# Kernel optimization log

Hardware: AMD Instinct MI355X
Metric: run time of the kernel (lower is better)

Reference implementation:

```python
import jax, jax.numpy as jnp
import numpy as np

N_NODES = 20000
N_EDGES = 320000
IN_CH = 64
OUT_CH = 64
HEADS = 4
NEG_SLOPE = 0.2
BN_EPS = 1e-5


def setup_inputs() -> dict:
    key = jax.random.key(0)
    ks = jax.random.split(key, 12)
    x = jax.random.normal(ks[0], (N_NODES, IN_CH), dtype=jnp.float32)
    embedding = jax.random.normal(ks[1], (N_NODES, OUT_CH), dtype=jnp.float32)
    # random edges guaranteed to have no self loops (module removes them anyway)
    src = jax.random.randint(ks[2], (N_EDGES,), 0, N_NODES, dtype=jnp.int32)
    off = jax.random.randint(ks[3], (N_EDGES,), 1, N_NODES, dtype=jnp.int32)
    dst = (src + off) % N_NODES
    edge_index = jnp.stack([src, dst], axis=0)  # [2, E]
    glorot = lambda k, shape: jax.random.uniform(k, shape, jnp.float32, -1.0, 1.0) * np.sqrt(6.0 / (shape[-2] * shape[-1] if len(shape) > 1 else shape[-1]))
    W = glorot(ks[4], (IN_CH, HEADS * OUT_CH))            # lin weight (no bias)
    att_i = glorot(ks[5], (1, HEADS, OUT_CH))
    att_j = glorot(ks[6], (1, HEADS, OUT_CH))
    att_em_i = glorot(ks[7], (1, HEADS, OUT_CH)) * 0.1    # zeros at init; random for test coverage
    att_em_j = glorot(ks[8], (1, HEADS, OUT_CH)) * 0.1
    bias = jnp.zeros((OUT_CH,), jnp.float32)
    gamma = jnp.ones((OUT_CH,), jnp.float32)
    beta = jnp.zeros((OUT_CH,), jnp.float32)
    return {"x": x, "edge_index": edge_index, "embedding": embedding, "W": W,
            "att_i": att_i, "att_j": att_j, "att_em_i": att_em_i, "att_em_j": att_em_j,
            "bias": bias, "gamma": gamma, "beta": beta}


def _gnn_forward(x, edge_index, embedding, W, att_i, att_j, att_em_i, att_em_j,
                 bias, gamma, beta):
    N = x.shape[0]
    H, C = att_i.shape[1], att_i.shape[2]
    # add self loops (input edges contain none by construction)
    loops = jnp.arange(N, dtype=edge_index.dtype)
    src = jnp.concatenate([edge_index[0], loops])  # x_j / embedding_j index
    dst = jnp.concatenate([edge_index[1], loops])  # x_i / embedding_i index (edge_index_i)
    xl = (x @ W).reshape(N, H, C)                  # [N,H,C]
    # attention logits decompose per node: <x, att> + <emb, att_em>
    logit_i = jnp.einsum('nhc,hc->nh', xl, att_i[0]) + jnp.einsum('nc,hc->nh', embedding, att_em_i[0])
    logit_j = jnp.einsum('nhc,hc->nh', xl, att_j[0]) + jnp.einsum('nc,hc->nh', embedding, att_em_j[0])
    alpha = logit_i[dst] + logit_j[src]            # [Etot,H]
    alpha = jnp.where(alpha >= 0, alpha, NEG_SLOPE * alpha)  # leaky_relu
    # segment softmax over destination node (PyG softmax)
    amax = jax.ops.segment_max(alpha, dst, num_segments=N)   # every node has a self loop
    alpha = jnp.exp(alpha - amax[dst])
    denom = jax.ops.segment_sum(alpha, dst, num_segments=N)
    alpha = alpha / (denom[dst] + 1e-16)
    # weighted message aggregation (scatter-add)
    msg = alpha[:, :, None] * xl[src]              # [Etot,H,C]
    out = jax.ops.segment_sum(msg, dst, num_segments=N)      # [N,H,C]
    out = out.mean(axis=1) + bias                  # concat=False -> head mean
    # BatchNorm1d (training-mode batch statistics) + ReLU
    mu = out.mean(axis=0)
    var = jnp.mean((out - mu) ** 2, axis=0)
    out = (out - mu) * jax.lax.rsqrt(var + BN_EPS) * gamma + beta
    return jax.nn.relu(out)


def reference(x, edge_index, embedding, W, att_i, att_j, att_em_i, att_em_j, bias, gamma, beta):
    return _gnn_forward(x, edge_index, embedding, W, att_i, att_j, att_em_i, att_em_j, bias, gamma, beta)
```

## Files before the change

kernel.cpp:

```cpp
#include <hip/hip_runtime.h>
#include <hip/hip_fp16.h>
#include <math.h>

#define N_NODES 20000
#define N_EDGES 320000
#define N_TOT (N_EDGES + N_NODES)
#define IN_CH 64
#define OUT_CH 64
#define HEADS 4
#define HC (HEADS * OUT_CH)
#define NEG_SLOPE 0.2f
#define BN_EPS 1e-5f
#define BN_SLOTS 64
#define CAP 64
#define XL_BLOCKS (N_NODES / 16)

__global__ __launch_bounds__(256) void k_xl(
    const float* __restrict__ x, const float* __restrict__ W,
    const float* __restrict__ emb, const float* __restrict__ att_i,
    const float* __restrict__ att_j, const float* __restrict__ att_em_i,
    const float* __restrict__ att_em_j, const int* __restrict__ srcA,
    const int* __restrict__ dstA, __half* __restrict__ xlh,
    float* __restrict__ logit_i, float* __restrict__ logit_j,
    int* __restrict__ cnt, int* __restrict__ bS, float* __restrict__ bnp) {
    __shared__ float xs[16][64];
    const int t = threadIdx.x;
    const int lane = t & 63, w = t >> 6;
    const int node0 = blockIdx.x * 16;
    const int gtid = blockIdx.x * 256 + t;

    if (gtid < BN_SLOTS * 128) bnp[gtid] = 0.f;

    {
        int n = t >> 4, c4 = (t & 15) * 4;
        float4 v = *(const float4*)&x[(node0 + n) * IN_CH + c4];
        *(float4*)&xs[n][c4] = v;
    }
    const float ai = att_i[t], aj = att_j[t];
    const float aei = att_em_i[t], aej = att_em_j[t];
    __syncthreads();

    const unsigned B = (unsigned)cnt[N_NODES];
    int s0, d0, p0;
    {
        const int e0 = gtid;
        if (e0 < N_EDGES) {
            s0 = srcA[e0];
            d0 = dstA[e0];
        } else {
            s0 = d0 = e0 - N_EDGES;
        }
        p0 = atomicAdd(&cnt[d0], 1);
    }
    const bool has1 = (gtid < N_TOT - XL_BLOCKS * 256);
    int p1 = 0;
    if (has1) p1 = atomicAdd(&cnt[gtid], 1);

    float acc[16];
#pragma unroll
    for (int n = 0; n < 16; ++n) acc[n] = 0.f;
#pragma unroll 1
    for (int kt = 0; kt < 4; ++kt) {
        float wt[16];
#pragma unroll
        for (int k = 0; k < 16; ++k) wt[k] = W[(kt * 16 + k) * HC + t];
#pragma unroll
        for (int n = 0; n < 16; ++n) {
            const float4* xr = (const float4*)&xs[n][kt * 16];
#pragma unroll
            for (int k4 = 0; k4 < 4; ++k4) {
                float4 xv = xr[k4];
                acc[n] += xv.x * wt[4 * k4] + xv.y * wt[4 * k4 + 1] +
                          xv.z * wt[4 * k4 + 2] + xv.w * wt[4 * k4 + 3];
            }
        }
    }

#pragma unroll
    for (int n = 0; n < 16; ++n) {
        const int gn = node0 + n;
        xlh[gn * HC + t] = __float2half(acc[n]);
        float e = emb[gn * OUT_CH + lane];
        float li = acc[n] * ai + e * aei;
        float lj = acc[n] * aj + e * aej;
#pragma unroll
        for (int o = 32; o > 0; o >>= 1) {
            li += __shfl_xor(li, o, 64);
            lj += __shfl_xor(lj, o, 64);
        }
        if (lane == 0) {
            logit_i[gn * HEADS + w] = li;
            logit_j[gn * HEADS + w] = lj;
        }
    }

    {
        unsigned pos = (unsigned)p0 - B;
        if (pos < CAP) bS[d0 * CAP + (int)pos] = s0;
    }
    if (has1) {
        unsigned pos = (unsigned)p1 - B;
        if (pos < CAP) bS[gtid * CAP + (int)pos] = gtid;
    }
}

__global__ __launch_bounds__(256) void k_node(
    const __half* __restrict__ xlh, const int* __restrict__ cnt,
    const int* __restrict__ bS, const float* __restrict__ logit_i,
    const float* __restrict__ logit_j, const float* __restrict__ bias,
    float* __restrict__ tmp, float* __restrict__ bnp) {
    const int t = threadIdx.x;
    const int wv = t >> 6, lane = t & 63;
    const int n = blockIdx.x * 4 + wv;
    const unsigned B = (unsigned)cnt[N_NODES];
    const int m = min((int)((unsigned)cnt[n] - B), CAP);
    const int h = lane >> 4;
    const int nb = n * CAP;
    const float li = logit_i[n * HEADS + h];

    float4 acc = {0.f, 0.f, 0.f, 0.f};
    float ssum = 0.f;

#pragma unroll 8
    for (int i = 0; i < m; ++i) {
        int s = bS[nb + i];
        float a = li + logit_j[s * HEADS + h];
        a = (a >= 0.f) ? a : NEG_SLOPE * a;
        float wgt = __expf(a);
        ushort4 r = *(const ushort4*)(xlh + (size_t)s * HC + lane * 4);
        ssum += wgt;
        acc.x += wgt * __half2float(__ushort_as_half(r.x));
        acc.y += wgt * __half2float(__ushort_as_half(r.y));
        acc.z += wgt * __half2float(__ushort_as_half(r.z));
        acc.w += wgt * __half2float(__ushort_as_half(r.w));
    }
    const float inv = 1.f / ssum;
    acc.x *= inv; acc.y *= inv; acc.z *= inv; acc.w *= inv;
#pragma unroll
    for (int o = 16; o <= 32; o <<= 1) {
        acc.x += __shfl_xor(acc.x, o, 64);
        acc.y += __shfl_xor(acc.y, o, 64);
        acc.z += __shfl_xor(acc.z, o, 64);
        acc.w += __shfl_xor(acc.w, o, 64);
    }
    __shared__ float rows[4][64];
    if (lane < 16) {
        int c = lane * 4;
        float4 b = *(const float4*)&bias[c];
        float4 o4 = {0.25f * acc.x + b.x, 0.25f * acc.y + b.y,
                     0.25f * acc.z + b.z, 0.25f * acc.w + b.w};
        *(float4*)&tmp[n * OUT_CH + c] = o4;
        *(float4*)&rows[wv][c] = o4;
    }
    __syncthreads();
    if (t < 64) {
        float s = 0.f, ss = 0.f;
#pragma unroll
        for (int r = 0; r < 4; ++r) {
            float v = rows[r][t];
            s += v;
            ss += v * v;
        }
        int slot = (blockIdx.x & (BN_SLOTS - 1)) * 128;
        atomicAdd(&bnp[slot + t], s);
        atomicAdd(&bnp[slot + 64 + t], ss);
    }
}

__global__ __launch_bounds__(256) void k_final(const float* __restrict__ tmp,
                                               const float* __restrict__ bnp,
                                               const float* __restrict__ gamma,
                                               const float* __restrict__ beta,
                                               float* __restrict__ out) {
    __shared__ float sscale[64], sshift[64];
    const int t = threadIdx.x;
    if (t < 64) {
        float s = 0.f, ss = 0.f;
#pragma unroll
        for (int k = 0; k < BN_SLOTS; ++k) {
            s += bnp[k * 128 + t];
            ss += bnp[k * 128 + 64 + t];
        }
        const float invN = 1.f / (float)N_NODES;
        float mu = s * invN;
        float var = ss * invN - mu * mu;
        float sc = rsqrtf(var + BN_EPS) * gamma[t];
        sscale[t] = sc;
        sshift[t] = beta[t] - mu * sc;
    }
    __syncthreads();
    const float4* t4 = (const float4*)tmp;
    float4* o4 = (float4*)out;
    const int total4 = N_NODES * OUT_CH / 4;
    for (int i = blockIdx.x * 256 + t; i < total4; i += gridDim.x * 256) {
        int c = (i & 15) * 4;
        float4 v = t4[i];
        float4 r;
        r.x = fmaxf(v.x * sscale[c] + sshift[c], 0.f);
        r.y = fmaxf(v.y * sscale[c + 1] + sshift[c + 1], 0.f);
        r.z = fmaxf(v.z * sscale[c + 2] + sshift[c + 2], 0.f);
        r.w = fmaxf(v.w * sscale[c + 3] + sshift[c + 3], 0.f);
        o4[i] = r;
    }
}

extern "C" void kernel_launch(void* const* d_in, const int* in_sizes, int n_in,
                              void* d_out, int out_size, void* d_ws,
                              size_t ws_size, hipStream_t stream) {
    const float* x = (const float*)d_in[0];
    const int* ei = (const int*)d_in[1];
    const float* emb = (const float*)d_in[2];
    const float* W = (const float*)d_in[3];
    const float* att_i = (const float*)d_in[4];
    const float* att_j = (const float*)d_in[5];
    const float* att_em_i = (const float*)d_in[6];
    const float* att_em_j = (const float*)d_in[7];
    const float* bias = (const float*)d_in[8];
    const float* gamma = (const float*)d_in[9];
    const float* beta = (const float*)d_in[10];
    float* out = (float*)d_out;

    const int* srcA = ei;
    const int* dstA = ei + N_EDGES;

    char* p = (char*)d_ws;
    auto alloc = [&](size_t bytes) {
        char* r = p;
        p += (bytes + 255) & ~size_t(255);
        return r;
    };
    __half* xlh = (__half*)alloc(sizeof(__half) * N_NODES * HC);
    float* lgi = (float*)alloc(sizeof(float) * N_NODES * HEADS);
    float* lgj = (float*)alloc(sizeof(float) * N_NODES * HEADS);
    float* tmp = (float*)alloc(sizeof(float) * N_NODES * OUT_CH);
    float* bnp = (float*)alloc(sizeof(float) * BN_SLOTS * 128);
    int* cnt = (int*)alloc(sizeof(int) * (N_NODES + 1));
    int* bS = (int*)alloc(sizeof(int) * N_NODES * CAP);
    (void)alloc(4096);

    k_xl<<<XL_BLOCKS, 256, 0, stream>>>(x, W, emb, att_i, att_j, att_em_i,
                                        att_em_j, srcA, dstA, xlh, lgi, lgj,
                                        cnt, bS, bnp);
    k_node<<<N_NODES / 4, 256, 0, stream>>>(xlh, cnt, bS, lgi, lgj, bias, tmp,
                                            bnp);
    k_final<<<256, 256, 0, stream>>>(tmp, bnp, gamma, beta, out);
}
```

Measured before the change: 162.6 us.

## Replicate edge-bucket counters across block groups to cut atomic contention

```diff
diff --git a/kernel.cpp b/kernel.cpp
--- a/kernel.cpp
+++ b/kernel.cpp
@@ -12,7 +12,9 @@
 #define NEG_SLOPE 0.2f
 #define BN_EPS 1e-5f
 #define BN_SLOTS 64
-#define CAP 64
+#define NREP 8
+#define SUBCAP 16
+#define CSTRIDE (N_NODES + 1)
 #define XL_BLOCKS (N_NODES / 16)
 
 __global__ __launch_bounds__(256) void k_xl(
@@ -28,6 +30,8 @@
     const int lane = t & 63, w = t >> 6;
     const int node0 = blockIdx.x * 16;
     const int gtid = blockIdx.x * 256 + t;
+    const int rid = blockIdx.x & (NREP - 1);
+    int* __restrict__ cntR = cnt + rid * CSTRIDE;
 
     if (gtid < BN_SLOTS * 128) bnp[gtid] = 0.f;
 
@@ -39,22 +43,6 @@
     const float ai = att_i[t], aj = att_j[t];
     const float aei = att_em_i[t], aej = att_em_j[t];
     __syncthreads();
-
-    const unsigned B = (unsigned)cnt[N_NODES];
-    int s0, d0, p0;
-    {
-        const int e0 = gtid;
-        if (e0 < N_EDGES) {
-            s0 = srcA[e0];
-            d0 = dstA[e0];
-        } else {
-            s0 = d0 = e0 - N_EDGES;
-        }
-        p0 = atomicAdd(&cnt[d0], 1);
-    }
-    const bool has1 = (gtid < N_TOT - XL_BLOCKS * 256);
-    int p1 = 0;
-    if (has1) p1 = atomicAdd(&cnt[gtid], 1);
 
     float acc[16];
 #pragma unroll
@@ -75,6 +63,17 @@
             }
         }
     }
+
+    const unsigned B = (unsigned)cntR[N_NODES];
+    int s0, d0, p0;
+    {
+        s0 = srcA[gtid];
+        d0 = dstA[gtid];
+        p0 = atomicAdd(&cntR[d0], 1);
+    }
+    const bool has1 = (gtid < N_NODES);
+    int p1 = 0;
+    if (has1) p1 = atomicAdd(&cntR[gtid], 1);
 
 #pragma unroll
     for (int n = 0; n < 16; ++n) {
@@ -96,11 +95,13 @@
 
     {
         unsigned pos = (unsigned)p0 - B;
-        if (pos < CAP) bS[d0 * CAP + (int)pos] = s0;
+        if (pos < SUBCAP)
+            bS[(d0 * NREP + rid) * SUBCAP + (int)pos] = s0;
     }
     if (has1) {
         unsigned pos = (unsigned)p1 - B;
-        if (pos < CAP) bS[gtid * CAP + (int)pos] = gtid;
+        if (pos < SUBCAP)
+            bS[(gtid * NREP + rid) * SUBCAP + (int)pos] = gtid;
     }
 }
 
@@ -112,27 +113,30 @@
     const int t = threadIdx.x;
     const int wv = t >> 6, lane = t & 63;
     const int n = blockIdx.x * 4 + wv;
-    const unsigned B = (unsigned)cnt[N_NODES];
-    const int m = min((int)((unsigned)cnt[n] - B), CAP);
     const int h = lane >> 4;
-    const int nb = n * CAP;
     const float li = logit_i[n * HEADS + h];
 
     float4 acc = {0.f, 0.f, 0.f, 0.f};
     float ssum = 0.f;
 
-#pragma unroll 8
-    for (int i = 0; i < m; ++i) {
-        int s = bS[nb + i];
-        float a = li + logit_j[s * HEADS + h];
-        a = (a >= 0.f) ? a : NEG_SLOPE * a;
-        float wgt = __expf(a);
-        ushort4 r = *(const ushort4*)(xlh + (size_t)s * HC + lane * 4);
-        ssum += wgt;
-        acc.x += wgt * __half2float(__ushort_as_half(r.x));
-        acc.y += wgt * __half2float(__ushort_as_half(r.y));
-        acc.z += wgt * __half2float(__ushort_as_half(r.z));
-        acc.w += wgt * __half2float(__ushort_as_half(r.w));
+#pragma unroll 1
+    for (int r = 0; r < NREP; ++r) {
+        const int cbase = r * CSTRIDE;
+        const unsigned B = (unsigned)cnt[cbase + N_NODES];
+        const int m = min((int)((unsigned)cnt[cbase + n] - B), SUBCAP);
+        const int nb = (n * NREP + r) * SUBCAP;
+        for (int i = 0; i < m; ++i) {
+            int s = bS[nb + i];
+            float a = li + logit_j[s * HEADS + h];
+            a = (a >= 0.f) ? a : NEG_SLOPE * a;
+            float wgt = __expf(a);
+            ushort4 rr = *(const ushort4*)(xlh + (size_t)s * HC + lane * 4);
+            ssum += wgt;
+            acc.x += wgt * __half2float(__ushort_as_half(rr.x));
+            acc.y += wgt * __half2float(__ushort_as_half(rr.y));
+            acc.z += wgt * __half2float(__ushort_as_half(rr.z));
+            acc.w += wgt * __half2float(__ushort_as_half(rr.w));
+        }
     }
     const float inv = 1.f / ssum;
     acc.x *= inv; acc.y *= inv; acc.z *= inv; acc.w *= inv;
@@ -234,8 +238,8 @@
     float* lgj = (float*)alloc(sizeof(float) * N_NODES * HEADS);
     float* tmp = (float*)alloc(sizeof(float) * N_NODES * OUT_CH);
     float* bnp = (float*)alloc(sizeof(float) * BN_SLOTS * 128);
-    int* cnt = (int*)alloc(sizeof(int) * (N_NODES + 1));
-    int* bS = (int*)alloc(sizeof(int) * N_NODES * CAP);
+    int* cnt = (int*)alloc(sizeof(int) * NREP * CSTRIDE);
+    int* bS = (int*)alloc(sizeof(int) * N_NODES * NREP * SUBCAP);
     (void)alloc(4096);
 
     k_xl<<<XL_BLOCKS, 256, 0, stream>>>(x, W, emb, att_i, att_j, att_em_i,
```

After: 181.5 us. +11.6%, slower.

## Halve nodes per block in projection kernel and move edge atomics after GEMM

Applied to the files above, without the earlier changes.

```diff
diff --git a/kernel.cpp b/kernel.cpp
--- a/kernel.cpp
+++ b/kernel.cpp
@@ -13,7 +13,8 @@
 #define BN_EPS 1e-5f
 #define BN_SLOTS 64
 #define CAP 64
-#define XL_BLOCKS (N_NODES / 16)
+#define NPB 8
+#define XL_BLOCKS (N_NODES / NPB)
 
 __global__ __launch_bounds__(256) void k_xl(
     const float* __restrict__ x, const float* __restrict__ W,
@@ -23,15 +24,15 @@
     const int* __restrict__ dstA, __half* __restrict__ xlh,
     float* __restrict__ logit_i, float* __restrict__ logit_j,
     int* __restrict__ cnt, int* __restrict__ bS, float* __restrict__ bnp) {
-    __shared__ float xs[16][64];
+    __shared__ float xs[NPB][64];
     const int t = threadIdx.x;
     const int lane = t & 63, w = t >> 6;
-    const int node0 = blockIdx.x * 16;
+    const int node0 = blockIdx.x * NPB;
     const int gtid = blockIdx.x * 256 + t;
 
     if (gtid < BN_SLOTS * 128) bnp[gtid] = 0.f;
 
-    {
+    if (t < NPB * 16) {
         int n = t >> 4, c4 = (t & 15) * 4;
         float4 v = *(const float4*)&x[(node0 + n) * IN_CH + c4];
         *(float4*)&xs[n][c4] = v;
@@ -40,32 +41,16 @@
     const float aei = att_em_i[t], aej = att_em_j[t];
     __syncthreads();
 
-    const unsigned B = (unsigned)cnt[N_NODES];
-    int s0, d0, p0;
-    {
-        const int e0 = gtid;
-        if (e0 < N_EDGES) {
-            s0 = srcA[e0];
-            d0 = dstA[e0];
-        } else {
-            s0 = d0 = e0 - N_EDGES;
-        }
-        p0 = atomicAdd(&cnt[d0], 1);
-    }
-    const bool has1 = (gtid < N_TOT - XL_BLOCKS * 256);
-    int p1 = 0;
-    if (has1) p1 = atomicAdd(&cnt[gtid], 1);
-
-    float acc[16];
-#pragma unroll
-    for (int n = 0; n < 16; ++n) acc[n] = 0.f;
+    float acc[NPB];
+#pragma unroll
+    for (int n = 0; n < NPB; ++n) acc[n] = 0.f;
 #pragma unroll 1
     for (int kt = 0; kt < 4; ++kt) {
         float wt[16];
 #pragma unroll
         for (int k = 0; k < 16; ++k) wt[k] = W[(kt * 16 + k) * HC + t];
 #pragma unroll
-        for (int n = 0; n < 16; ++n) {
+        for (int n = 0; n < NPB; ++n) {
             const float4* xr = (const float4*)&xs[n][kt * 16];
 #pragma unroll
             for (int k4 = 0; k4 < 4; ++k4) {
@@ -76,8 +61,21 @@
         }
     }
 
-#pragma unroll
-    for (int n = 0; n < 16; ++n) {
+    const unsigned B = (unsigned)cnt[N_NODES];
+    const bool hasE = (gtid < N_TOT);
+    int s0 = 0, d0 = 0, p0 = 0;
+    if (hasE) {
+        if (gtid < N_EDGES) {
+            s0 = srcA[gtid];
+            d0 = dstA[gtid];
+        } else {
+            s0 = d0 = gtid - N_EDGES;
+        }
+        p0 = atomicAdd(&cnt[d0], 1);
+    }
+
+#pragma unroll
+    for (int n = 0; n < NPB; ++n) {
         const int gn = node0 + n;
         xlh[gn * HC + t] = __float2half(acc[n]);
         float e = emb[gn * OUT_CH + lane];
@@ -94,13 +92,9 @@
         }
     }
 
-    {
+    if (hasE) {
         unsigned pos = (unsigned)p0 - B;
         if (pos < CAP) bS[d0 * CAP + (int)pos] = s0;
-    }
-    if (has1) {
-        unsigned pos = (unsigned)p1 - B;
-        if (pos < CAP) bS[gtid * CAP + (int)pos] = gtid;
     }
 }
 
```

Result: faster. 150.9 us (-7.2%).
